# Kernel optimization log

Measured on AMD Instinct MI355X. Metric: run time of the kernel, lower is better.

Reference implementation:

```python
import jax, jax.numpy as jnp
import numpy as np

B, N, F, Tf, Tm, Df, Dm = 8, 128, 128, 64, 256, 32, 128
E, H, TE = 64, 128, 64  # node_emb_dim, hidden_dim, time_emb_dim


def setup_inputs() -> dict:
    key = jax.random.key(0)
    ks = jax.random.split(key, 16)
    s = 0.05
    return {
        'noisy_adj': jax.random.normal(ks[0], (B, N, N), jnp.float32),
        'node_feats': jax.random.normal(ks[1], (B, N, F), jnp.float32),
        'feat_fnirs': jax.random.normal(ks[2], (B, N, Tf, Df), jnp.float32),
        'feat_music': jax.random.normal(ks[3], (B, 1, Tm, Dm), jnp.float32),
        'g_pre': jax.random.normal(ks[4], (B, N, N), jnp.float32),
        'node_W': jax.random.normal(ks[5], (F, E), jnp.float32) * s,
        'node_b': jnp.zeros((E,), jnp.float32),
        'fnirs_W': jax.random.normal(ks[6], (Df, H), jnp.float32) * s,
        'fnirs_b': jnp.zeros((H,), jnp.float32),
        'music_W': jax.random.normal(ks[7], (Dm, H), jnp.float32) * s,
        'music_b': jnp.zeros((H,), jnp.float32),
        'mlp_W1': jax.random.normal(ks[8], (2 * E + 2 + H + TE, H), jnp.float32) * s,
        'mlp_b1': jnp.zeros((H,), jnp.float32),
        'mlp_W2': jax.random.normal(ks[9], (H, 1), jnp.float32) * s,
        'mlp_b2': jnp.zeros((1,), jnp.float32),
        't': jax.random.randint(ks[10], (B,), 0, Tf),
    }


def _time_embedding(t_idx):
    # sinusoidal timestep embedding -> [B, TE]
    half = TE // 2
    inv_freq = jnp.exp(-jnp.arange(half, dtype=jnp.float32) * (jnp.log(10000.0) / (half - 1)))
    freqs = t_idx.astype(jnp.float32)[:, None] * inv_freq  # [B, half]
    return jnp.concatenate([jnp.sin(freqs), jnp.cos(freqs)], axis=-1)


def _conditional(feat_fnirs, feat_music, fnirs_W, fnirs_b, music_W, music_b):
    # cross-attention: fNIRS timesteps attend over music timesteps
    q = feat_fnirs @ fnirs_W + fnirs_b          # [B,N,Tf,H]
    kv = feat_music @ music_W + music_b         # [B,1,Tm,H]
    scale = 1.0 / jnp.sqrt(jnp.float32(H))
    scores = jnp.einsum('bnfh,bomh->bnfm', q, kv) * scale  # [B,N,Tf,Tm]
    attn = jax.nn.softmax(scores, axis=-1)
    ctx = jnp.einsum('bnfm,bomh->bnfh', attn, kv)
    fused = q + ctx                              # [B,N,Tf,H]
    attn_weights = attn.mean(axis=1)             # mean across channels -> [B,Tf,Tm]
    ent = -(attn * jnp.log(attn + 1e-8)).sum(-1)
    attention_loss = ent.mean()
    return fused, attn_weights, attention_loss


def reference(noisy_adj, node_feats, feat_fnirs, feat_music, g_pre,
              node_W, node_b, fnirs_W, fnirs_b, music_W, music_b,
              mlp_W1, mlp_b1, mlp_W2, mlp_b2, t):
    h = node_feats @ node_W + node_b             # [B,N,E]

    fused, attn_weights, attention_loss = _conditional(
        feat_fnirs, feat_music, fnirs_W, fnirs_b, music_W, music_b)

    t_idx = jnp.clip(t, 0, fused.shape[2] - 1)
    # gather conditional state at diffusion step t -> [B,N,H]
    idx = jnp.broadcast_to(t_idx[:, None, None, None], (B, N, 1, H))
    cond_t = jnp.take_along_axis(fused, idx, axis=2)[:, :, 0, :]

    time_emb = _time_embedding(t_idx)            # [B,TE]

    # Fused edge MLP layer-1: split W1 along the concat axis instead of
    # materializing the [B,N,N,in_dim] concat tensor (same math).
    W1_hi = mlp_W1[:E]
    W1_hj = mlp_W1[E:2 * E]
    w_adj = mlp_W1[2 * E]          # [H]
    w_gpre = mlp_W1[2 * E + 1]     # [H]
    W1_cond = mlp_W1[2 * E + 2:2 * E + 2 + H]
    W1_time = mlp_W1[2 * E + 2 + H:]

    pre = ((h @ W1_hi)[:, :, None, :]            # h_i varies over row i
           + (h @ W1_hj)[:, None, :, :]          # h_j varies over col j
           + noisy_adj[..., None] * w_adj
           + g_pre[..., None] * w_gpre
           + (cond_t @ W1_cond)[:, None, :, :]   # cond broadcast over row i
           + (time_emb @ W1_time)[:, None, None, :]
           + mlp_b1)                             # [B,N,N,H]
    hid = jax.nn.relu(pre)
    noise_pred = (hid @ mlp_W2)[..., 0] + mlp_b2[0]  # [B,N,N]
    return noise_pred, attn_weights, attention_loss
```

## Files before the change

### kernel.cpp

```cpp
#include <hip/hip_runtime.h>
#include <hip/hip_bf16.h>

#define Bn  8
#define Nn  128
#define Fn  128
#define Tfn 64
#define Tmn 256
#define Dfn 32
#define Dmn 128
#define En  64
#define Hn  128
#define TEn 64

#define OUT_AW_OFF   (Bn*Nn*Nn)
#define OUT_LOSS_OFF (Bn*Nn*Nn + Bn*Tfn*Tmn)

#define WS_G     0
#define WS_BIAS  32768
#define WS_KVT   34816
#define WS_FWT   165888
#define WS_NWT   167936
#define WS_HIT   172032
#define WS_HJT   176128
#define WS_CONDT 180224
#define WS_TVEC  188416
#define WS_PI    189440
#define WS_PJ    320512
#define WS_LOSS  451584
#define WS_MWT   451588
#define WS_FWB   459780

#define SCALE 0.08838834764831845f

typedef __attribute__((ext_vector_type(8))) short short8;
typedef __attribute__((ext_vector_type(4))) float f32x4;

__device__ __forceinline__ unsigned short f2bf(float x) {
  __hip_bfloat16 h = __float2bfloat16(x);
  return __builtin_bit_cast(unsigned short, h);
}
__device__ __forceinline__ unsigned int pk2(float a, float b) {
  return (unsigned int)f2bf(a) | ((unsigned int)f2bf(b) << 16);
}

__global__ __launch_bounds__(128) void k_wprep(
    const float* __restrict__ W1, const float* __restrict__ b1,
    const float* __restrict__ node_W, const float* __restrict__ fnirs_W,
    const float* __restrict__ fnirs_b, const float* __restrict__ music_W,
    const int* __restrict__ t,
    unsigned short* __restrict__ fwt, unsigned short* __restrict__ nwt,
    unsigned short* __restrict__ hit, unsigned short* __restrict__ hjt,
    unsigned short* __restrict__ condt, unsigned short* __restrict__ mwt,
    unsigned short* __restrict__ fwb, float* __restrict__ tvec,
    float* __restrict__ loss_acc)
{
  int blk = blockIdx.x, tid = threadIdx.x;
  if (blk < 8) {
    int b = blk;
    __shared__ float te_l[TEn];
    if (tid < TEn/2) {
      int tcl = min(max(t[b], 0), Tfn - 1);
      float fr = (float)tcl * __expf(-(float)tid * (logf(10000.f) / (TEn/2 - 1)));
      te_l[tid] = __sinf(fr);
      te_l[tid + TEn/2] = __cosf(fr);
    }
    __syncthreads();
    float a = b1[tid];
    #pragma unroll 8
    for (int u = 0; u < TEn; u++) a = fmaf(te_l[u], W1[(2*En + 2 + Hn + u)*Hn + tid], a);
    tvec[b*Hn + tid] = a;
    if (b == 0 && tid == 0) loss_acc[0] = 0.f;
  } else if (blk < 16) {
    int q = blk - 8;
    #pragma unroll 4
    for (int i = 0; i < 16; i++) {
      int k = q*16 + i;
      condt[k*Hn + tid] = f2bf(W1[(2*En + 2 + tid)*Hn + k]);
    }
  } else if (blk < 20) {
    int q = blk - 16;
    int e = tid & 63, kh = tid >> 6;
    #pragma unroll 4
    for (int i = 0; i < 16; i++) {
      int k = q*32 + kh*16 + i;
      hit[k*En + e] = f2bf(W1[e*Hn + k]);
    }
  } else if (blk < 24) {
    int q = blk - 20;
    int e = tid & 63, kh = tid >> 6;
    #pragma unroll 4
    for (int i = 0; i < 16; i++) {
      int k = q*32 + kh*16 + i;
      hjt[k*En + e] = f2bf(W1[(En + e)*Hn + k]);
    }
  } else if (blk < 32) {
    int q = blk - 24;
    int fl = tid & 15, eh = tid >> 4;
    #pragma unroll 4
    for (int i = 0; i < 8; i++) {
      int e = eh*8 + i;
      nwt[e*Fn + q*16 + fl] = f2bf(node_W[(q*16 + fl)*En + e]);
    }
  } else if (blk < 34) {
    int q = blk - 32;
    int d = tid & 31, hh = tid >> 5;
    #pragma unroll 4
    for (int i = 0; i < 16; i++) {
      int h = q*64 + hh*16 + i;
      fwt[h*Dfn + d] = f2bf(fnirs_W[d*Hn + h]);
    }
  } else if (blk < 36) {
    int q = blk - 34;
    #pragma unroll 4
    for (int i = 0; i < 64; i++) {
      int h = q*64 + i;
      mwt[h*Dmn + tid] = f2bf(music_W[(size_t)tid*Hn + h]);
    }
  } else {
    #pragma unroll 4
    for (int row = 0; row < 48; row++) {
      float v = (row < 32) ? fnirs_W[row*Hn + tid] : (row == 32 ? fnirs_b[tid] : 0.f);
      fwb[row*Hn + tid] = f2bf(v);
    }
  }
}

__global__ __launch_bounds__(256) void k_music(
    const float* __restrict__ feat_music, const float* __restrict__ music_b,
    const unsigned short* __restrict__ mwt, const unsigned short* __restrict__ fwb,
    unsigned short* __restrict__ kvT, unsigned short* __restrict__ G_bf,
    float* __restrict__ bias)
{
  __shared__ unsigned short fm_l[32][136];
  __shared__ unsigned short kv_l[32][136];

  int tid = threadIdx.x;
  int b = blockIdx.x >> 3;
  int m0 = (blockIdx.x & 7) << 5;

  {
    int m = tid >> 3, c = (tid & 7) * 16;
    const float* src = feat_music + ((size_t)b*Tmn + m0 + m)*Dmn + c;
    float4 x0 = ((const float4*)src)[0];
    float4 x1 = ((const float4*)src)[1];
    float4 x2 = ((const float4*)src)[2];
    float4 x3 = ((const float4*)src)[3];
    uint4 pa, pb;
    pa.x = pk2(x0.x, x0.y); pa.y = pk2(x0.z, x0.w);
    pa.z = pk2(x1.x, x1.y); pa.w = pk2(x1.z, x1.w);
    pb.x = pk2(x2.x, x2.y); pb.y = pk2(x2.z, x2.w);
    pb.z = pk2(x3.x, x3.y); pb.w = pk2(x3.z, x3.w);
    uint4* dst = (uint4*)&fm_l[m][c];
    dst[0] = pa; dst[1] = pb;
  }
  __syncthreads();

  int lane = tid & 63, wv = tid >> 6;
  int col = lane & 15, kq = lane >> 4;
  int rt = wv & 1, cp = wv >> 1;

  short8 aF[4];
  #pragma unroll
  for (int ks = 0; ks < 4; ks++)
    aF[ks] = *(const short8*)&fm_l[rt*16 + col][ks*32 + kq*8];

  #pragma unroll
  for (int htl = 0; htl < 4; htl++) {
    int ht = cp*4 + htl;
    int h = ht*16 + col;
    f32x4 acc = {0.f,0.f,0.f,0.f};
    #pragma unroll
    for (int ks = 0; ks < 4; ks++) {
      short8 bfr = *(const short8*)(mwt + (size_t)h*Dmn + ks*32 + kq*8);
      acc = __builtin_amdgcn_mfma_f32_16x16x32_bf16(aF[ks], bfr, acc, 0, 0, 0);
    }
    float mb = music_b[h];
    unsigned short kvb[4];
    #pragma unroll
    for (int r = 0; r < 4; r++) {
      float v = acc[r] + mb;
      kvb[r] = f2bf(v);
      kv_l[rt*16 + kq*4 + r][h] = kvb[r];
    }
    *(ushort4*)(kvT + ((size_t)b*Hn + h)*Tmn + m0 + rt*16 + kq*4) =
        make_ushort4(kvb[0], kvb[1], kvb[2], kvb[3]);
  }
  __syncthreads();

  short8 aK[4];
  #pragma unroll
  for (int ks = 0; ks < 4; ks++)
    aK[ks] = *(const short8*)&kv_l[rt*16 + col][ks*32 + kq*8];

  int nct = (cp == 0) ? 2 : 1;
  for (int cti = 0; cti < nct; cti++) {
    int ct = (cp == 0) ? cti*2 : 1;
    f32x4 acc = {0.f,0.f,0.f,0.f};
    #pragma unroll
    for (int ks = 0; ks < 4; ks++) {
      short8 bfr = *(const short8*)(fwb + (size_t)(ct*16 + col)*Hn + ks*32 + kq*8);
      acc = __builtin_amdgcn_mfma_f32_16x16x32_bf16(aK[ks], bfr, acc, 0, 0, 0);
    }
    if (ct < 2) {
      #pragma unroll
      for (int r = 0; r < 4; r++)
        G_bf[((size_t)b*Tmn + m0 + rt*16 + kq*4 + r)*Dfn + ct*16 + col] =
            f2bf(acc[r] * SCALE);
    } else if (col == 0) {
      #pragma unroll
      for (int r = 0; r < 4; r++)
        bias[(size_t)b*Tmn + m0 + rt*16 + kq*4 + r] = acc[r] * SCALE;
    }
  }
}

struct SmemAttn {
  unsigned short feat_l[Nn][40];
  unsigned short G_l[Tmn][40];
  float bias_l[Tmn];
  float aw_l[4][Tmn];
  float ent_l[4];
};
struct SmemCond {
  unsigned short featT_l[16][40];
  unsigned short A_l[16][264];
  unsigned short nf_l[16][136];
  unsigned short h_l[16][72];
  unsigned short cond_l[16][136];
  float sS[4][16];
  float tvec_l[Hn];
};
union __align__(16) SmemK2 {
  SmemAttn a;
  SmemCond c;
};

__global__ __launch_bounds__(256, 2) void k_attn_cond(
    const float* __restrict__ feat_fnirs, const float* __restrict__ node_feats,
    const float* __restrict__ node_b, const int* __restrict__ t,
    const unsigned short* __restrict__ G_bf, const float* __restrict__ bias,
    const unsigned short* __restrict__ kvT, const unsigned short* __restrict__ fwt,
    const unsigned short* __restrict__ nwt, const unsigned short* __restrict__ hit,
    const unsigned short* __restrict__ hjt, const unsigned short* __restrict__ condt,
    const float* __restrict__ tvec, float* __restrict__ Pi, float* __restrict__ Pj,
    float* __restrict__ aw_out, float* __restrict__ loss_acc)
{
  __shared__ SmemK2 smem;
  int tid = threadIdx.x;
  int lane = tid & 63, wv = tid >> 6;
  int col = lane & 15, kq = lane >> 4;

  if (blockIdx.x < 512) {
    int b = blockIdx.x >> 6, f = blockIdx.x & 63;
    {
      const uint4* gg = (const uint4*)(G_bf + (size_t)b*Tmn*Dfn);
      #pragma unroll
      for (int v0 = 0; v0 < 4; v0++) {
        int v = tid + v0*256;
        uint4 x = gg[v];
        int m = v >> 2, qt = v & 3;
        *((uint4*)&smem.a.G_l[m][qt*8]) = x;
      }
      smem.a.bias_l[tid] = bias[b*Tmn + tid];
      int n = tid >> 1, hf = tid & 1;
      const float* src = feat_fnirs + (((size_t)b*Nn + n)*Tfn + f)*Dfn + hf*16;
      float4 x0 = ((const float4*)src)[0];
      float4 x1 = ((const float4*)src)[1];
      float4 x2 = ((const float4*)src)[2];
      float4 x3 = ((const float4*)src)[3];
      uint4 pa, pb;
      pa.x = pk2(x0.x, x0.y); pa.y = pk2(x0.z, x0.w);
      pa.z = pk2(x1.x, x1.y); pa.w = pk2(x1.z, x1.w);
      pb.x = pk2(x2.x, x2.y); pb.y = pk2(x2.z, x2.w);
      pb.z = pk2(x3.x, x3.y); pb.w = pk2(x3.z, x3.w);
      uint4* dst = (uint4*)&smem.a.feat_l[n][hf*16];
      dst[0] = pa; dst[1] = pb;
    }
    __syncthreads();

    int n0 = wv * 32;
    short8 a0 = *(const short8*)&smem.a.feat_l[n0 + col][kq*8];
    short8 a1 = *(const short8*)&smem.a.feat_l[n0 + 16 + col][kq*8];

    float S0[4] = {0,0,0,0}, S1[4] = {0,0,0,0};
    float T0[4] = {0,0,0,0}, T1[4] = {0,0,0,0};
    float p0[16][4], p1[16][4];

    #pragma unroll
    for (int mt = 0; mt < 16; mt++) {
      short8 bfr = *(const short8*)&smem.a.G_l[mt*16 + col][kq*8];
      float bv = smem.a.bias_l[mt*16 + col];
      f32x4 c0 = __builtin_amdgcn_mfma_f32_16x16x32_bf16(a0, bfr, (f32x4){0.f,0.f,0.f,0.f}, 0, 0, 0);
      f32x4 c1 = __builtin_amdgcn_mfma_f32_16x16x32_bf16(a1, bfr, (f32x4){0.f,0.f,0.f,0.f}, 0, 0, 0);
      #pragma unroll
      for (int r = 0; r < 4; r++) {
        float sc = c0[r] + bv;
        float p = __expf(sc);
        S0[r] += p; T0[r] = fmaf(p, sc, T0[r]); p0[mt][r] = p;
        sc = c1[r] + bv;
        p = __expf(sc);
        S1[r] += p; T1[r] = fmaf(p, sc, T1[r]); p1[mt][r] = p;
      }
    }

    #pragma unroll
    for (int r = 0; r < 4; r++) {
      #pragma unroll
      for (int off = 1; off < 16; off <<= 1) {
        S0[r] += __shfl_xor(S0[r], off);
        S1[r] += __shfl_xor(S1[r], off);
        T0[r] += __shfl_xor(T0[r], off);
        T1[r] += __shfl_xor(T1[r], off);
      }
    }
    float i0v[4], i1v[4];
    #pragma unroll
    for (int r = 0; r < 4; r++) { i0v[r] = 1.f / S0[r]; i1v[r] = 1.f / S1[r]; }

    float ent = 0.f;
    if (col == 0) {
      #pragma unroll
      for (int r = 0; r < 4; r++) {
        ent += (__logf(S0[r]) - T0[r] * i0v[r]);
        ent += (__logf(S1[r]) - T1[r] * i1v[r]);
      }
    }
    ent += __shfl_xor(ent, 32); ent += __shfl_xor(ent, 16);
    ent += __shfl_xor(ent, 8);  ent += __shfl_xor(ent, 4);
    ent += __shfl_xor(ent, 2);  ent += __shfl_xor(ent, 1);
    if (lane == 0) smem.a.ent_l[wv] = ent;

    #pragma unroll
    for (int mt = 0; mt < 16; mt++) {
      float a = 0.f;
      #pragma unroll
      for (int r = 0; r < 4; r++) {
        a = fmaf(p0[mt][r], i0v[r], a);
        a = fmaf(p1[mt][r], i1v[r], a);
      }
      a += __shfl_xor(a, 16);
      a += __shfl_xor(a, 32);
      if (lane < 16) smem.a.aw_l[wv][mt*16 + lane] = a;
    }
    __syncthreads();

    float s = (smem.a.aw_l[0][tid] + smem.a.aw_l[1][tid]) +
              (smem.a.aw_l[2][tid] + smem.a.aw_l[3][tid]);
    aw_out[((size_t)b*Tfn + f)*Tmn + tid] = s * (1.f/(float)Nn);
    if (tid == 0)
      atomicAdd(loss_acc, (smem.a.ent_l[0] + smem.a.ent_l[1]) +
                          (smem.a.ent_l[2] + smem.a.ent_l[3]));
    return;
  }

  int blk = blockIdx.x - 512;
  int b = blk >> 3;
  int i0 = (blk & 7) << 4;
  int tcl = min(max(t[b], 0), Tfn - 1);

  if (tid < 128) {
    int i = tid >> 3, c = (tid & 7) * 4;
    const float* src = feat_fnirs + (((size_t)b*Nn + i0 + i)*Tfn + tcl)*Dfn + c;
    float4 x = *(const float4*)src;
    *(unsigned int*)&smem.c.featT_l[i][c]     = pk2(x.x, x.y);
    *(unsigned int*)&smem.c.featT_l[i][c + 2] = pk2(x.z, x.w);
    smem.c.tvec_l[tid] = tvec[b*Hn + tid];
  }
  {
    int i = tid >> 4, c = (tid & 15) * 8;
    const float* src = node_feats + ((size_t)b*Nn + i0 + i)*Fn + c;
    float4 x0 = ((const float4*)src)[0];
    float4 x1 = ((const float4*)src)[1];
    *(unsigned int*)&smem.c.nf_l[i][c]     = pk2(x0.x, x0.y);
    *(unsigned int*)&smem.c.nf_l[i][c + 2] = pk2(x0.z, x0.w);
    *(unsigned int*)&smem.c.nf_l[i][c + 4] = pk2(x1.x, x1.y);
    *(unsigned int*)&smem.c.nf_l[i][c + 6] = pk2(x1.z, x1.w);
  }
  __syncthreads();

  short8 a_feat = *(const short8*)&smem.c.featT_l[col][kq*8];

  float p[4][4];
  float Sp[4] = {0,0,0,0};
  #pragma unroll
  for (int mtl = 0; mtl < 4; mtl++) {
    int mt = wv*4 + mtl;
    short8 bg = *(const short8*)(G_bf + ((size_t)b*Tmn + mt*16 + col)*Dfn + kq*8);
    f32x4 c = __builtin_amdgcn_mfma_f32_16x16x32_bf16(a_feat, bg, (f32x4){0.f,0.f,0.f,0.f}, 0, 0, 0);
    float bv = bias[b*Tmn + mt*16 + col];
    #pragma unroll
    for (int r = 0; r < 4; r++) {
      float pp = __expf(c[r] + bv);
      p[mtl][r] = pp;
      Sp[r] += pp;
    }
  }
  #pragma unroll
  for (int r = 0; r < 4; r++) {
    float v = Sp[r];
    v += __shfl_xor(v, 1); v += __shfl_xor(v, 2);
    v += __shfl_xor(v, 4); v += __shfl_xor(v, 8);
    Sp[r] = v;
  }
  if (col == 0) {
    #pragma unroll
    for (int r = 0; r < 4; r++) smem.c.sS[wv][kq*4 + r] = Sp[r];
  }
  __syncthreads();
  float invS[4];
  #pragma unroll
  for (int r = 0; r < 4; r++)
    invS[r] = 1.f / (smem.c.sS[0][kq*4+r] + smem.c.sS[1][kq*4+r] +
                     smem.c.sS[2][kq*4+r] + smem.c.sS[3][kq*4+r]);
  #pragma unroll
  for (int mtl = 0; mtl < 4; mtl++) {
    #pragma unroll
    for (int r = 0; r < 4; r++)
      smem.c.A_l[kq*4 + r][(wv*4 + mtl)*16 + col] = f2bf(p[mtl][r] * invS[r]);
  }
  __syncthreads();

  f32x4 accC0 = {0.f,0.f,0.f,0.f}, accC1 = {0.f,0.f,0.f,0.f};
  {
    int ct0 = wv*2, ct1 = wv*2 + 1;
    short8 bq0 = *(const short8*)(fwt + (size_t)(ct0*16 + col)*Dfn + kq*8);
    short8 bq1 = *(const short8*)(fwt + (size_t)(ct1*16 + col)*Dfn + kq*8);
    accC0 = __builtin_amdgcn_mfma_f32_16x16x32_bf16(a_feat, bq0, accC0, 0, 0, 0);
    accC1 = __builtin_amdgcn_mfma_f32_16x16x32_bf16(a_feat, bq1, accC1, 0, 0, 0);
    #pragma unroll
    for (int ks = 0; ks < 8; ks++) {
      short8 aA = *(const short8*)&smem.c.A_l[col][ks*32 + kq*8];
      short8 bk0 = *(const short8*)(kvT + ((size_t)b*Hn + ct0*16 + col)*Tmn + ks*32 + kq*8);
      short8 bk1 = *(const short8*)(kvT + ((size_t)b*Hn + ct1*16 + col)*Tmn + ks*32 + kq*8);
      accC0 = __builtin_amdgcn_mfma_f32_16x16x32_bf16(aA, bk0, accC0, 0, 0, 0);
      accC1 = __builtin_amdgcn_mfma_f32_16x16x32_bf16(aA, bk1, accC1, 0, 0, 0);
    }
  }
  f32x4 accH = {0.f,0.f,0.f,0.f};
  #pragma unroll
  for (int ks = 0; ks < 4; ks++) {
    short8 aN = *(const short8*)&smem.c.nf_l[col][ks*32 + kq*8];
    short8 bn = *(const short8*)(nwt + (size_t)(wv*16 + col)*Fn + ks*32 + kq*8);
    accH = __builtin_amdgcn_mfma_f32_16x16x32_bf16(aN, bn, accH, 0, 0, 0);
  }
  float nb = node_b[wv*16 + col];
  #pragma unroll
  for (int r = 0; r < 4; r++) {
    smem.c.cond_l[kq*4 + r][(wv*2    )*16 + col] = f2bf(accC0[r]);
    smem.c.cond_l[kq*4 + r][(wv*2 + 1)*16 + col] = f2bf(accC1[r]);
    smem.c.h_l[kq*4 + r][wv*16 + col] = f2bf(accH[r] + nb);
  }
  __syncthreads();

  short8 aH[2];
  aH[0] = *(const short8*)&smem.c.h_l[col][kq*8];
  aH[1] = *(const short8*)&smem.c.h_l[col][32 + kq*8];
  #pragma unroll
  for (int ctl = 0; ctl < 2; ctl++) {
    int ct = wv*2 + ctl;
    f32x4 accPi = {0.f,0.f,0.f,0.f}, accPj = {0.f,0.f,0.f,0.f};
    #pragma unroll
    for (int ks = 0; ks < 2; ks++) {
      short8 bi_ = *(const short8*)(hit + (size_t)(ct*16 + col)*En + ks*32 + kq*8);
      short8 bj_ = *(const short8*)(hjt + (size_t)(ct*16 + col)*En + ks*32 + kq*8);
      accPi = __builtin_amdgcn_mfma_f32_16x16x32_bf16(aH[ks], bi_, accPi, 0, 0, 0);
      accPj = __builtin_amdgcn_mfma_f32_16x16x32_bf16(aH[ks], bj_, accPj, 0, 0, 0);
    }
    #pragma unroll
    for (int ks = 0; ks < 4; ks++) {
      short8 aC = *(const short8*)&smem.c.cond_l[col][ks*32 + kq*8];
      short8 bc = *(const short8*)(condt + (size_t)(ct*16 + col)*Hn + ks*32 + kq*8);
      accPj = __builtin_amdgcn_mfma_f32_16x16x32_bf16(aC, bc, accPj, 0, 0, 0);
    }
    float tv = smem.c.tvec_l[ct*16 + col];
    #pragma unroll
    for (int r = 0; r < 4; r++) {
      size_t row = (size_t)b*Nn + i0 + kq*4 + r;
      Pi[row*Hn + ct*16 + col] = accPi[r];
      Pj[row*Hn + ct*16 + col] = accPj[r] + tv;
    }
  }
}

__global__ __launch_bounds__(256) void k_edge(
    const float* __restrict__ adj, const float* __restrict__ gpre,
    const float* __restrict__ W1, const float* __restrict__ W2,
    const float* __restrict__ b2p, const float* __restrict__ Pi,
    const float* __restrict__ Pj, float* __restrict__ out,
    const float* __restrict__ loss_acc)
{
  int b  = blockIdx.x >> 6;
  int ib = (blockIdx.x >> 1) & 31;
  int jh = blockIdx.x & 1;
  int i0 = ib * 4;
  int tid = threadIdx.x;

  __shared__ float4 Pj_s4[64*32];
  __shared__ float4 Pi_s4[4*32];
  __shared__ float4 w2_s[32], wa_s[32], wg_s[32];

  {
    const float4* Pjg = (const float4*)(Pj + ((size_t)b*Nn + jh*64)*Hn);
    #pragma unroll
    for (int v0 = 0; v0 < 8; v0++) {
      int idx = tid + v0*256;
      int j = idx >> 5, c = idx & 31;
      Pj_s4[j*32 + (c ^ (j & 31))] = Pjg[j*32 + c];
    }
    if (tid < 128) {
      int r = tid >> 5, c = tid & 31;
      Pi_s4[r*32 + c] = ((const float4*)(Pi + ((size_t)b*Nn + i0 + r)*Hn))[c];
    } else if (tid < 160) {
      int c = tid - 128;
      w2_s[c] = ((const float4*)W2)[c];
      wa_s[c] = ((const float4*)(W1 + (2*En)*Hn))[c];
      wg_s[c] = ((const float4*)(W1 + (2*En + 1)*Hn))[c];
    }
  }
  __syncthreads();

  int r = tid >> 6, lane = tid & 63;
  int i = i0 + r, j = jh*64 + lane;
  float b2v = b2p[0];
  float adjv = adj [((size_t)b*Nn + i)*Nn + j];
  float gpv  = gpre[((size_t)b*Nn + i)*Nn + j];
  float a0 = 0.f, a1 = 0.f, a2 = 0.f, a3 = 0.f;
  #pragma unroll
  for (int c = 0; c < 32; c++) {
    float4 pj = Pj_s4[lane*32 + (c ^ (lane & 31))];
    float4 pi = Pi_s4[r*32 + c];
    float4 wa = wa_s[c], wg = wg_s[c], w2 = w2_s[c];
    float e0 = pi.x + pj.x + adjv*wa.x + gpv*wg.x;
    float e1 = pi.y + pj.y + adjv*wa.y + gpv*wg.y;
    float e2 = pi.z + pj.z + adjv*wa.z + gpv*wg.z;
    float e3 = pi.w + pj.w + adjv*wa.w + gpv*wg.w;
    a0 = fmaf(fmaxf(e0, 0.f), w2.x, a0);
    a1 = fmaf(fmaxf(e1, 0.f), w2.y, a1);
    a2 = fmaf(fmaxf(e2, 0.f), w2.z, a2);
    a3 = fmaf(fmaxf(e3, 0.f), w2.w, a3);
  }
  out[((size_t)b*Nn + i)*Nn + j] = (a0 + a1) + (a2 + a3) + b2v;

  if (blockIdx.x == 0 && tid == 0)
    out[OUT_LOSS_OFF] = loss_acc[0] * (1.f / (float)(Bn*Nn*Tfn));
}

extern "C" void kernel_launch(void* const* d_in, const int* in_sizes, int n_in,
                              void* d_out, int out_size, void* d_ws, size_t ws_size,
                              hipStream_t stream) {
  (void)in_sizes; (void)n_in; (void)out_size; (void)ws_size;
  const float* noisy_adj  = (const float*)d_in[0];
  const float* node_feats = (const float*)d_in[1];
  const float* feat_fnirs = (const float*)d_in[2];
  const float* feat_music = (const float*)d_in[3];
  const float* g_pre      = (const float*)d_in[4];
  const float* node_W     = (const float*)d_in[5];
  const float* node_b     = (const float*)d_in[6];
  const float* fnirs_W    = (const float*)d_in[7];
  const float* fnirs_b    = (const float*)d_in[8];
  const float* music_W    = (const float*)d_in[9];
  const float* music_b    = (const float*)d_in[10];
  const float* mlp_W1     = (const float*)d_in[11];
  const float* mlp_b1     = (const float*)d_in[12];
  const float* mlp_W2     = (const float*)d_in[13];
  const float* mlp_b2     = (const float*)d_in[14];
  const int*   t          = (const int*)d_in[15];

  float* out = (float*)d_out;
  float* ws = (float*)d_ws;
  unsigned short* g_ws    = (unsigned short*)(ws + WS_G);
  float*          bias_ws = ws + WS_BIAS;
  unsigned short* kvt_ws  = (unsigned short*)(ws + WS_KVT);
  unsigned short* fwt_ws  = (unsigned short*)(ws + WS_FWT);
  unsigned short* nwt_ws  = (unsigned short*)(ws + WS_NWT);
  unsigned short* hit_ws  = (unsigned short*)(ws + WS_HIT);
  unsigned short* hjt_ws  = (unsigned short*)(ws + WS_HJT);
  unsigned short* cndt_ws = (unsigned short*)(ws + WS_CONDT);
  float*          tvec_ws = ws + WS_TVEC;
  float*          Pi_ws   = ws + WS_PI;
  float*          Pj_ws   = ws + WS_PJ;
  float*          loss_ws = ws + WS_LOSS;
  unsigned short* mwt_ws  = (unsigned short*)(ws + WS_MWT);
  unsigned short* fwb_ws  = (unsigned short*)(ws + WS_FWB);

  k_wprep    <<<37,   128, 0, stream>>>(mlp_W1, mlp_b1, node_W, fnirs_W, fnirs_b,
                                        music_W, t, fwt_ws, nwt_ws, hit_ws, hjt_ws,
                                        cndt_ws, mwt_ws, fwb_ws, tvec_ws, loss_ws);
  k_music    <<<64,   256, 0, stream>>>(feat_music, music_b, mwt_ws, fwb_ws,
                                        kvt_ws, g_ws, bias_ws);
  k_attn_cond<<<576,  256, 0, stream>>>(feat_fnirs, node_feats, node_b, t,
                                        g_ws, bias_ws, kvt_ws, fwt_ws, nwt_ws,
                                        hit_ws, hjt_ws, cndt_ws, tvec_ws,
                                        Pi_ws, Pj_ws, out + OUT_AW_OFF, loss_ws);
  k_edge     <<<512,  256, 0, stream>>>(noisy_adj, g_pre, mlp_W1, mlp_W2, mlp_b2,
                                        Pi_ws, Pj_ws, out, loss_ws);
}
```

Before: 136.5 us.

## Fuse all four kernels into one persistent kernel with grid barriers

Replaces the four separate launches (weight prep, music projection, attention/cond, edge MLP) with one 256-block kernel that uses atomic-counter grid barriers between phases. The music and fnirs weight transposes are dropped, and those weights are converted to bf16 on the fly inside the music phase. Each block now loops over two attention units and over later-phase work. This removes launch overhead and the inter-kernel gaps. In exchange it adds spin-wait barriers, which rely on all 256 blocks being co-resident, plus a memset, and there are strided scalar loads of music_W.

```diff
diff --git a/kernel.cpp b/kernel.cpp
--- a/kernel.cpp
+++ b/kernel.cpp
@@ -27,8 +27,6 @@
 #define WS_PI    189440
 #define WS_PJ    320512
 #define WS_LOSS  451584
-#define WS_MWT   451588
-#define WS_FWB   459780
 
 #define SCALE 0.08838834764831845f
 
@@ -43,175 +41,15 @@
   return (unsigned int)f2bf(a) | ((unsigned int)f2bf(b) << 16);
 }
 
-__global__ __launch_bounds__(128) void k_wprep(
-    const float* __restrict__ W1, const float* __restrict__ b1,
-    const float* __restrict__ node_W, const float* __restrict__ fnirs_W,
-    const float* __restrict__ fnirs_b, const float* __restrict__ music_W,
-    const int* __restrict__ t,
-    unsigned short* __restrict__ fwt, unsigned short* __restrict__ nwt,
-    unsigned short* __restrict__ hit, unsigned short* __restrict__ hjt,
-    unsigned short* __restrict__ condt, unsigned short* __restrict__ mwt,
-    unsigned short* __restrict__ fwb, float* __restrict__ tvec,
-    float* __restrict__ loss_acc)
-{
-  int blk = blockIdx.x, tid = threadIdx.x;
-  if (blk < 8) {
-    int b = blk;
-    __shared__ float te_l[TEn];
-    if (tid < TEn/2) {
-      int tcl = min(max(t[b], 0), Tfn - 1);
-      float fr = (float)tcl * __expf(-(float)tid * (logf(10000.f) / (TEn/2 - 1)));
-      te_l[tid] = __sinf(fr);
-      te_l[tid + TEn/2] = __cosf(fr);
-    }
-    __syncthreads();
-    float a = b1[tid];
-    #pragma unroll 8
-    for (int u = 0; u < TEn; u++) a = fmaf(te_l[u], W1[(2*En + 2 + Hn + u)*Hn + tid], a);
-    tvec[b*Hn + tid] = a;
-    if (b == 0 && tid == 0) loss_acc[0] = 0.f;
-  } else if (blk < 16) {
-    int q = blk - 8;
-    #pragma unroll 4
-    for (int i = 0; i < 16; i++) {
-      int k = q*16 + i;
-      condt[k*Hn + tid] = f2bf(W1[(2*En + 2 + tid)*Hn + k]);
-    }
-  } else if (blk < 20) {
-    int q = blk - 16;
-    int e = tid & 63, kh = tid >> 6;
-    #pragma unroll 4
-    for (int i = 0; i < 16; i++) {
-      int k = q*32 + kh*16 + i;
-      hit[k*En + e] = f2bf(W1[e*Hn + k]);
-    }
-  } else if (blk < 24) {
-    int q = blk - 20;
-    int e = tid & 63, kh = tid >> 6;
-    #pragma unroll 4
-    for (int i = 0; i < 16; i++) {
-      int k = q*32 + kh*16 + i;
-      hjt[k*En + e] = f2bf(W1[(En + e)*Hn + k]);
-    }
-  } else if (blk < 32) {
-    int q = blk - 24;
-    int fl = tid & 15, eh = tid >> 4;
-    #pragma unroll 4
-    for (int i = 0; i < 8; i++) {
-      int e = eh*8 + i;
-      nwt[e*Fn + q*16 + fl] = f2bf(node_W[(q*16 + fl)*En + e]);
-    }
-  } else if (blk < 34) {
-    int q = blk - 32;
-    int d = tid & 31, hh = tid >> 5;
-    #pragma unroll 4
-    for (int i = 0; i < 16; i++) {
-      int h = q*64 + hh*16 + i;
-      fwt[h*Dfn + d] = f2bf(fnirs_W[d*Hn + h]);
-    }
-  } else if (blk < 36) {
-    int q = blk - 34;
-    #pragma unroll 4
-    for (int i = 0; i < 64; i++) {
-      int h = q*64 + i;
-      mwt[h*Dmn + tid] = f2bf(music_W[(size_t)tid*Hn + h]);
-    }
-  } else {
-    #pragma unroll 4
-    for (int row = 0; row < 48; row++) {
-      float v = (row < 32) ? fnirs_W[row*Hn + tid] : (row == 32 ? fnirs_b[tid] : 0.f);
-      fwb[row*Hn + tid] = f2bf(v);
-    }
-  }
-}
-
-__global__ __launch_bounds__(256) void k_music(
-    const float* __restrict__ feat_music, const float* __restrict__ music_b,
-    const unsigned short* __restrict__ mwt, const unsigned short* __restrict__ fwb,
-    unsigned short* __restrict__ kvT, unsigned short* __restrict__ G_bf,
-    float* __restrict__ bias)
-{
-  __shared__ unsigned short fm_l[32][136];
-  __shared__ unsigned short kv_l[32][136];
-
-  int tid = threadIdx.x;
-  int b = blockIdx.x >> 3;
-  int m0 = (blockIdx.x & 7) << 5;
-
-  {
-    int m = tid >> 3, c = (tid & 7) * 16;
-    const float* src = feat_music + ((size_t)b*Tmn + m0 + m)*Dmn + c;
-    float4 x0 = ((const float4*)src)[0];
-    float4 x1 = ((const float4*)src)[1];
-    float4 x2 = ((const float4*)src)[2];
-    float4 x3 = ((const float4*)src)[3];
-    uint4 pa, pb;
-    pa.x = pk2(x0.x, x0.y); pa.y = pk2(x0.z, x0.w);
-    pa.z = pk2(x1.x, x1.y); pa.w = pk2(x1.z, x1.w);
-    pb.x = pk2(x2.x, x2.y); pb.y = pk2(x2.z, x2.w);
-    pb.z = pk2(x3.x, x3.y); pb.w = pk2(x3.z, x3.w);
-    uint4* dst = (uint4*)&fm_l[m][c];
-    dst[0] = pa; dst[1] = pb;
+__device__ __forceinline__ void grid_barrier(unsigned int* ctr, unsigned int target) {
+  __syncthreads();
+  __threadfence();
+  if (threadIdx.x == 0) {
+    atomicAdd(ctr, 1u);
+    while (atomicAdd(ctr, 0u) < target) __builtin_amdgcn_s_sleep(8);
   }
   __syncthreads();
-
-  int lane = tid & 63, wv = tid >> 6;
-  int col = lane & 15, kq = lane >> 4;
-  int rt = wv & 1, cp = wv >> 1;
-
-  short8 aF[4];
-  #pragma unroll
-  for (int ks = 0; ks < 4; ks++)
-    aF[ks] = *(const short8*)&fm_l[rt*16 + col][ks*32 + kq*8];
-
-  #pragma unroll
-  for (int htl = 0; htl < 4; htl++) {
-    int ht = cp*4 + htl;
-    int h = ht*16 + col;
-    f32x4 acc = {0.f,0.f,0.f,0.f};
-    #pragma unroll
-    for (int ks = 0; ks < 4; ks++) {
-      short8 bfr = *(const short8*)(mwt + (size_t)h*Dmn + ks*32 + kq*8);
-      acc = __builtin_amdgcn_mfma_f32_16x16x32_bf16(aF[ks], bfr, acc, 0, 0, 0);
-    }
-    float mb = music_b[h];
-    unsigned short kvb[4];
-    #pragma unroll
-    for (int r = 0; r < 4; r++) {
-      float v = acc[r] + mb;
-      kvb[r] = f2bf(v);
-      kv_l[rt*16 + kq*4 + r][h] = kvb[r];
-    }
-    *(ushort4*)(kvT + ((size_t)b*Hn + h)*Tmn + m0 + rt*16 + kq*4) =
-        make_ushort4(kvb[0], kvb[1], kvb[2], kvb[3]);
-  }
-  __syncthreads();
-
-  short8 aK[4];
-  #pragma unroll
-  for (int ks = 0; ks < 4; ks++)
-    aK[ks] = *(const short8*)&kv_l[rt*16 + col][ks*32 + kq*8];
-
-  int nct = (cp == 0) ? 2 : 1;
-  for (int cti = 0; cti < nct; cti++) {
-    int ct = (cp == 0) ? cti*2 : 1;
-    f32x4 acc = {0.f,0.f,0.f,0.f};
-    #pragma unroll
-    for (int ks = 0; ks < 4; ks++) {
-      short8 bfr = *(const short8*)(fwb + (size_t)(ct*16 + col)*Hn + ks*32 + kq*8);
-      acc = __builtin_amdgcn_mfma_f32_16x16x32_bf16(aK[ks], bfr, acc, 0, 0, 0);
-    }
-    if (ct < 2) {
-      #pragma unroll
-      for (int r = 0; r < 4; r++)
-        G_bf[((size_t)b*Tmn + m0 + rt*16 + kq*4 + r)*Dfn + ct*16 + col] =
-            f2bf(acc[r] * SCALE);
-    } else if (col == 0) {
-      #pragma unroll
-      for (int r = 0; r < 4; r++)
-        bias[(size_t)b*Tmn + m0 + rt*16 + kq*4 + r] = acc[r] * SCALE;
-    }
-  }
+  __threadfence();
 }
 
 struct SmemAttn {
@@ -230,28 +68,228 @@
   float sS[4][16];
   float tvec_l[Hn];
 };
-union __align__(16) SmemK2 {
+struct SmemMusic {
+  unsigned short fm_l[32][136];
+  unsigned short kv_l[32][136];
+};
+struct SmemWprep { float te_l[TEn]; };
+struct SmemEdge {
+  float4 Pj_s4[64*32];
+  float4 Pi_s4[4*32];
+  float4 w2_s[32];
+  float4 wa_s[32];
+  float4 wg_s[32];
+};
+union __align__(16) SmemAll {
   SmemAttn a;
   SmemCond c;
+  SmemMusic m;
+  SmemWprep w;
+  SmemEdge e;
 };
 
-__global__ __launch_bounds__(256, 2) void k_attn_cond(
-    const float* __restrict__ feat_fnirs, const float* __restrict__ node_feats,
-    const float* __restrict__ node_b, const int* __restrict__ t,
-    const unsigned short* __restrict__ G_bf, const float* __restrict__ bias,
-    const unsigned short* __restrict__ kvT, const unsigned short* __restrict__ fwt,
-    const unsigned short* __restrict__ nwt, const unsigned short* __restrict__ hit,
-    const unsigned short* __restrict__ hjt, const unsigned short* __restrict__ condt,
-    const float* __restrict__ tvec, float* __restrict__ Pi, float* __restrict__ Pj,
-    float* __restrict__ aw_out, float* __restrict__ loss_acc)
+__global__ __launch_bounds__(256, 2) void k_all(
+    const float* __restrict__ noisy_adj, const float* __restrict__ node_feats,
+    const float* __restrict__ feat_fnirs, const float* __restrict__ feat_music,
+    const float* __restrict__ g_pre, const float* __restrict__ node_W,
+    const float* __restrict__ node_b, const float* __restrict__ fnirs_W,
+    const float* __restrict__ fnirs_b, const float* __restrict__ music_W,
+    const float* __restrict__ music_b, const float* __restrict__ W1,
+    const float* __restrict__ b1, const float* __restrict__ W2,
+    const float* __restrict__ b2p, const int* __restrict__ t,
+    float* __restrict__ out, float* __restrict__ ws)
 {
-  __shared__ SmemK2 smem;
+  __shared__ SmemAll smem;
+
+  unsigned short* G_bf  = (unsigned short*)(ws + WS_G);
+  float*          bias  = ws + WS_BIAS;
+  unsigned short* kvT   = (unsigned short*)(ws + WS_KVT);
+  unsigned short* fwt   = (unsigned short*)(ws + WS_FWT);
+  unsigned short* nwt   = (unsigned short*)(ws + WS_NWT);
+  unsigned short* hit   = (unsigned short*)(ws + WS_HIT);
+  unsigned short* hjt   = (unsigned short*)(ws + WS_HJT);
+  unsigned short* condt = (unsigned short*)(ws + WS_CONDT);
+  float*          tvec  = ws + WS_TVEC;
+  float*          Pi    = ws + WS_PI;
+  float*          Pj    = ws + WS_PJ;
+  float*          loss_acc = ws + WS_LOSS;
+  unsigned int*   bar1  = (unsigned int*)(ws + WS_LOSS + 1);
+  unsigned int*   bar2  = (unsigned int*)(ws + WS_LOSS + 2);
+  float*          aw_out   = out + OUT_AW_OFF;
+
   int tid = threadIdx.x;
+  int blk = blockIdx.x;
   int lane = tid & 63, wv = tid >> 6;
   int col = lane & 15, kq = lane >> 4;
 
-  if (blockIdx.x < 512) {
-    int b = blockIdx.x >> 6, f = blockIdx.x & 63;
+  if (blk < 64) {
+    int b = blk >> 3;
+    int m0 = (blk & 7) << 5;
+    {
+      int m = tid >> 3, c = (tid & 7) * 16;
+      const float* src = feat_music + ((size_t)b*Tmn + m0 + m)*Dmn + c;
+      float4 x0 = ((const float4*)src)[0];
+      float4 x1 = ((const float4*)src)[1];
+      float4 x2 = ((const float4*)src)[2];
+      float4 x3 = ((const float4*)src)[3];
+      uint4 pa, pb;
+      pa.x = pk2(x0.x, x0.y); pa.y = pk2(x0.z, x0.w);
+      pa.z = pk2(x1.x, x1.y); pa.w = pk2(x1.z, x1.w);
+      pb.x = pk2(x2.x, x2.y); pb.y = pk2(x2.z, x2.w);
+      pb.z = pk2(x3.x, x3.y); pb.w = pk2(x3.z, x3.w);
+      uint4* dst = (uint4*)&smem.m.fm_l[m][c];
+      dst[0] = pa; dst[1] = pb;
+    }
+    __syncthreads();
+    int rt = wv & 1, cp = wv >> 1;
+    short8 aF[4];
+    #pragma unroll
+    for (int ks = 0; ks < 4; ks++)
+      aF[ks] = *(const short8*)&smem.m.fm_l[rt*16 + col][ks*32 + kq*8];
+
+    #pragma unroll
+    for (int htl = 0; htl < 4; htl++) {
+      int h = (cp*4 + htl)*16 + col;
+      f32x4 acc = {0.f,0.f,0.f,0.f};
+      #pragma unroll
+      for (int ks = 0; ks < 4; ks++) {
+        int d0 = ks*32 + kq*8;
+        short8 bfr;
+        #pragma unroll
+        for (int j = 0; j < 8; j++)
+          bfr[j] = (short)f2bf(music_W[(size_t)(d0 + j)*Hn + h]);
+        acc = __builtin_amdgcn_mfma_f32_16x16x32_bf16(aF[ks], bfr, acc, 0, 0, 0);
+      }
+      float mb = music_b[h];
+      unsigned short kvb[4];
+      #pragma unroll
+      for (int r = 0; r < 4; r++) {
+        float v = acc[r] + mb;
+        kvb[r] = f2bf(v);
+        smem.m.kv_l[rt*16 + kq*4 + r][h] = kvb[r];
+      }
+      *(ushort4*)(kvT + ((size_t)b*Hn + h)*Tmn + m0 + rt*16 + kq*4) =
+          make_ushort4(kvb[0], kvb[1], kvb[2], kvb[3]);
+    }
+    __syncthreads();
+    short8 aK[4];
+    #pragma unroll
+    for (int ks = 0; ks < 4; ks++)
+      aK[ks] = *(const short8*)&smem.m.kv_l[rt*16 + col][ks*32 + kq*8];
+    int nct = (cp == 0) ? 2 : 1;
+    for (int cti = 0; cti < nct; cti++) {
+      int ct = (cp == 0) ? cti*2 : 1;
+      f32x4 acc = {0.f,0.f,0.f,0.f};
+      #pragma unroll
+      for (int ks = 0; ks < 4; ks++) {
+        int d0 = ks*32 + kq*8;
+        short8 bfr;
+        if (ct < 2) {
+          const float* wr = fnirs_W + (size_t)(ct*16 + col)*Hn + d0;
+          float4 wa = ((const float4*)wr)[0];
+          float4 wb = ((const float4*)wr)[1];
+          uint4 uu;
+          uu.x = pk2(wa.x, wa.y); uu.y = pk2(wa.z, wa.w);
+          uu.z = pk2(wb.x, wb.y); uu.w = pk2(wb.z, wb.w);
+          bfr = __builtin_bit_cast(short8, uu);
+        } else if (col == 0) {
+          const float* wr = fnirs_b + d0;
+          float4 wa = ((const float4*)wr)[0];
+          float4 wb = ((const float4*)wr)[1];
+          uint4 uu;
+          uu.x = pk2(wa.x, wa.y); uu.y = pk2(wa.z, wa.w);
+          uu.z = pk2(wb.x, wb.y); uu.w = pk2(wb.z, wb.w);
+          bfr = __builtin_bit_cast(short8, uu);
+        } else {
+          bfr = (short8){0,0,0,0,0,0,0,0};
+        }
+        acc = __builtin_amdgcn_mfma_f32_16x16x32_bf16(aK[ks], bfr, acc, 0, 0, 0);
+      }
+      if (ct < 2) {
+        #pragma unroll
+        for (int r = 0; r < 4; r++)
+          G_bf[((size_t)b*Tmn + m0 + rt*16 + kq*4 + r)*Dfn + ct*16 + col] =
+              f2bf(acc[r] * SCALE);
+      } else if (col == 0) {
+        #pragma unroll
+        for (int r = 0; r < 4; r++)
+          bias[(size_t)b*Tmn + m0 + rt*16 + kq*4 + r] = acc[r] * SCALE;
+      }
+    }
+  } else if (blk < 98) {
+    int wblk = blk - 64;
+    if (wblk < 8) {
+      int b = wblk;
+      if (tid < TEn/2) {
+        int tcl = min(max(t[b], 0), Tfn - 1);
+        float fr = (float)tcl * __expf(-(float)tid * (logf(10000.f) / (TEn/2 - 1)));
+        smem.w.te_l[tid] = __sinf(fr);
+        smem.w.te_l[tid + TEn/2] = __cosf(fr);
+      }
+      __syncthreads();
+      if (tid < Hn) {
+        float a = b1[tid];
+        #pragma unroll 8
+        for (int u = 0; u < TEn; u++)
+          a = fmaf(smem.w.te_l[u], W1[(2*En + 2 + Hn + u)*Hn + tid], a);
+        tvec[b*Hn + tid] = a;
+      }
+    } else if (wblk < 16) {
+      int q = wblk - 8;
+      if (tid < 128) {
+        #pragma unroll 4
+        for (int i = 0; i < 16; i++) {
+          int k = q*16 + i;
+          condt[k*Hn + tid] = f2bf(W1[(2*En + 2 + tid)*Hn + k]);
+        }
+      }
+    } else if (wblk < 20) {
+      int q = wblk - 16;
+      if (tid < 128) {
+        int e = tid & 63, kh = tid >> 6;
+        #pragma unroll 4
+        for (int i = 0; i < 16; i++) {
+          int k = q*32 + kh*16 + i;
+          hit[k*En + e] = f2bf(W1[e*Hn + k]);
+        }
+      }
+    } else if (wblk < 24) {
+      int q = wblk - 20;
+      if (tid < 128) {
+        int e = tid & 63, kh = tid >> 6;
+        #pragma unroll 4
+        for (int i = 0; i < 16; i++) {
+          int k = q*32 + kh*16 + i;
+          hjt[k*En + e] = f2bf(W1[(En + e)*Hn + k]);
+        }
+      }
+    } else if (wblk < 32) {
+      int q = wblk - 24;
+      if (tid < 128) {
+        int fl = tid & 15, eh = tid >> 4;
+        #pragma unroll 4
+        for (int i = 0; i < 8; i++) {
+          int e = eh*8 + i;
+          nwt[e*Fn + q*16 + fl] = f2bf(node_W[(q*16 + fl)*En + e]);
+        }
+      }
+    } else {
+      int q = wblk - 32;
+      if (tid < 128) {
+        int d = tid & 31, hh = tid >> 5;
+        #pragma unroll 4
+        for (int i = 0; i < 16; i++) {
+          int h = q*64 + hh*16 + i;
+          fwt[h*Dfn + d] = f2bf(fnirs_W[d*Hn + h]);
+        }
+      }
+    }
+  }
+  grid_barrier(bar1, 256);
+
+  for (int u = 0; u < 2; u++) {
+    int unit = blk*2 + u;
+    int b = unit >> 6, f = unit & 63;
     {
       const uint4* gg = (const uint4*)(G_bf + (size_t)b*Tmn*Dfn);
       #pragma unroll
@@ -350,198 +388,191 @@
     if (tid == 0)
       atomicAdd(loss_acc, (smem.a.ent_l[0] + smem.a.ent_l[1]) +
                           (smem.a.ent_l[2] + smem.a.ent_l[3]));
-    return;
+    __syncthreads();
   }
 
-  int blk = blockIdx.x - 512;
-  int b = blk >> 3;
-  int i0 = (blk & 7) << 4;
-  int tcl = min(max(t[b], 0), Tfn - 1);
-
-  if (tid < 128) {
-    int i = tid >> 3, c = (tid & 7) * 4;
-    const float* src = feat_fnirs + (((size_t)b*Nn + i0 + i)*Tfn + tcl)*Dfn + c;
-    float4 x = *(const float4*)src;
-    *(unsigned int*)&smem.c.featT_l[i][c]     = pk2(x.x, x.y);
-    *(unsigned int*)&smem.c.featT_l[i][c + 2] = pk2(x.z, x.w);
-    smem.c.tvec_l[tid] = tvec[b*Hn + tid];
+  if (blk < 64) {
+    int b = blk >> 3;
+    int i0 = (blk & 7) << 4;
+    int tcl = min(max(t[b], 0), Tfn - 1);
+
+    if (tid < 128) {
+      int i = tid >> 3, c = (tid & 7) * 4;
+      const float* src = feat_fnirs + (((size_t)b*Nn + i0 + i)*Tfn + tcl)*Dfn + c;
+      float4 x = *(const float4*)src;
+      *(unsigned int*)&smem.c.featT_l[i][c]     = pk2(x.x, x.y);
+      *(unsigned int*)&smem.c.featT_l[i][c + 2] = pk2(x.z, x.w);
+      smem.c.tvec_l[tid] = tvec[b*Hn + tid];
+    }
+    {
+      int i = tid >> 4, c = (tid & 15) * 8;
+      const float* src = node_feats + ((size_t)b*Nn + i0 + i)*Fn + c;
+      float4 x0 = ((const float4*)src)[0];
+      float4 x1 = ((const float4*)src)[1];
+      *(unsigned int*)&smem.c.nf_l[i][c]     = pk2(x0.x, x0.y);
+      *(unsigned int*)&smem.c.nf_l[i][c + 2] = pk2(x0.z, x0.w);
+      *(unsigned int*)&smem.c.nf_l[i][c + 4] = pk2(x1.x, x1.y);
+      *(unsigned int*)&smem.c.nf_l[i][c + 6] = pk2(x1.z, x1.w);
+    }
+    __syncthreads();
+
+    short8 a_feat = *(const short8*)&smem.c.featT_l[col][kq*8];
+
+    float p[4][4];
+    float Sp[4] = {0,0,0,0};
+    #pragma unroll
+    for (int mtl = 0; mtl < 4; mtl++) {
+      int mt = wv*4 + mtl;
+      short8 bg = *(const short8*)(G_bf + ((size_t)b*Tmn + mt*16 + col)*Dfn + kq*8);
+      f32x4 c = __builtin_amdgcn_mfma_f32_16x16x32_bf16(a_feat, bg, (f32x4){0.f,0.f,0.f,0.f}, 0, 0, 0);
+      float bv = bias[b*Tmn + mt*16 + col];
+      #pragma unroll
+      for (int r = 0; r < 4; r++) {
+        float pp = __expf(c[r] + bv);
+        p[mtl][r] = pp;
+        Sp[r] += pp;
+      }
+    }
+    #pragma unroll
+    for (int r = 0; r < 4; r++) {
+      float v = Sp[r];
+      v += __shfl_xor(v, 1); v += __shfl_xor(v, 2);
+      v += __shfl_xor(v, 4); v += __shfl_xor(v, 8);
+      Sp[r] = v;
+    }
+    if (col == 0) {
+      #pragma unroll
+      for (int r = 0; r < 4; r++) smem.c.sS[wv][kq*4 + r] = Sp[r];
+    }
+    __syncthreads();
+    float invS[4];
+    #pragma unroll
+    for (int r = 0; r < 4; r++)
+      invS[r] = 1.f / (smem.c.sS[0][kq*4+r] + smem.c.sS[1][kq*4+r] +
+                       smem.c.sS[2][kq*4+r] + smem.c.sS[3][kq*4+r]);
+    #pragma unroll
+    for (int mtl = 0; mtl < 4; mtl++) {
+      #pragma unroll
+      for (int r = 0; r < 4; r++)
+        smem.c.A_l[kq*4 + r][(wv*4 + mtl)*16 + col] = f2bf(p[mtl][r] * invS[r]);
+    }
+    __syncthreads();
+
+    f32x4 accC0 = {0.f,0.f,0.f,0.f}, accC1 = {0.f,0.f,0.f,0.f};
+    {
+      int ct0 = wv*2, ct1 = wv*2 + 1;
+      short8 bq0 = *(const short8*)(fwt + (size_t)(ct0*16 + col)*Dfn + kq*8);
+      short8 bq1 = *(const short8*)(fwt + (size_t)(ct1*16 + col)*Dfn + kq*8);
+      accC0 = __builtin_amdgcn_mfma_f32_16x16x32_bf16(a_feat, bq0, accC0, 0, 0, 0);
+      accC1 = __builtin_amdgcn_mfma_f32_16x16x32_bf16(a_feat, bq1, accC1, 0, 0, 0);
+      #pragma unroll
+      for (int ks = 0; ks < 8; ks++) {
+        short8 aA = *(const short8*)&smem.c.A_l[col][ks*32 + kq*8];
+        short8 bk0 = *(const short8*)(kvT + ((size_t)b*Hn + ct0*16 + col)*Tmn + ks*32 + kq*8);
+        short8 bk1 = *(const short8*)(kvT + ((size_t)b*Hn + ct1*16 + col)*Tmn + ks*32 + kq*8);
+        accC0 = __builtin_amdgcn_mfma_f32_16x16x32_bf16(aA, bk0, accC0, 0, 0, 0);
+        accC1 = __builtin_amdgcn_mfma_f32_16x16x32_bf16(aA, bk1, accC1, 0, 0, 0);
+      }
+    }
+    f32x4 accH = {0.f,0.f,0.f,0.f};
+    #pragma unroll
+    for (int ks = 0; ks < 4; ks++) {
+      short8 aN = *(const short8*)&smem.c.nf_l[col][ks*32 + kq*8];
+      short8 bn = *(const short8*)(nwt + (size_t)(wv*16 + col)*Fn + ks*32 + kq*8);
+      accH = __builtin_amdgcn_mfma_f32_16x16x32_bf16(aN, bn, accH, 0, 0, 0);
+    }
+    float nb = node_b[wv*16 + col];
+    #pragma unroll
+    for (int r = 0; r < 4; r++) {
+      smem.c.cond_l[kq*4 + r][(wv*2    )*16 + col] = f2bf(accC0[r]);
+      smem.c.cond_l[kq*4 + r][(wv*2 + 1)*16 + col] = f2bf(accC1[r]);
+      smem.c.h_l[kq*4 + r][wv*16 + col] = f2bf(accH[r] + nb);
+    }
+    __syncthreads();
+
+    short8 aH[2];
+    aH[0] = *(const short8*)&smem.c.h_l[col][kq*8];
+    aH[1] = *(const short8*)&smem.c.h_l[col][32 + kq*8];
+    #pragma unroll
+    for (int ctl = 0; ctl < 2; ctl++) {
+      int ct = wv*2 + ctl;
+      f32x4 accPi = {0.f,0.f,0.f,0.f}, accPj = {0.f,0.f,0.f,0.f};
+      #pragma unroll
+      for (int ks = 0; ks < 2; ks++) {
+        short8 bi_ = *(const short8*)(hit + (size_t)(ct*16 + col)*En + ks*32 + kq*8);
+        short8 bj_ = *(const short8*)(hjt + (size_t)(ct*16 + col)*En + ks*32 + kq*8);
+        accPi = __builtin_amdgcn_mfma_f32_16x16x32_bf16(aH[ks], bi_, accPi, 0, 0, 0);
+        accPj = __builtin_amdgcn_mfma_f32_16x16x32_bf16(aH[ks], bj_, accPj, 0, 0, 0);
+      }
+      #pragma unroll
+      for (int ks = 0; ks < 4; ks++) {
+        short8 aC = *(const short8*)&smem.c.cond_l[col][ks*32 + kq*8];
+        short8 bc = *(const short8*)(condt + (size_t)(ct*16 + col)*Hn + ks*32 + kq*8);
+        accPj = __builtin_amdgcn_mfma_f32_16x16x32_bf16(aC, bc, accPj, 0, 0, 0);
+      }
+      float tv = smem.c.tvec_l[ct*16 + col];
+      #pragma unroll
+      for (int r = 0; r < 4; r++) {
+        size_t row = (size_t)b*Nn + i0 + kq*4 + r;
+        Pi[row*Hn + ct*16 + col] = accPi[r];
+        Pj[row*Hn + ct*16 + col] = accPj[r] + tv;
+      }
+    }
   }
-  {
-    int i = tid >> 4, c = (tid & 15) * 8;
-    const float* src = node_feats + ((size_t)b*Nn + i0 + i)*Fn + c;
-    float4 x0 = ((const float4*)src)[0];
-    float4 x1 = ((const float4*)src)[1];
-    *(unsigned int*)&smem.c.nf_l[i][c]     = pk2(x0.x, x0.y);
-    *(unsigned int*)&smem.c.nf_l[i][c + 2] = pk2(x0.z, x0.w);
-    *(unsigned int*)&smem.c.nf_l[i][c + 4] = pk2(x1.x, x1.y);
-    *(unsigned int*)&smem.c.nf_l[i][c + 6] = pk2(x1.z, x1.w);
+  grid_barrier(bar2, 256);
+
+  for (int u = 0; u < 2; u++) {
+    int unit = blk*2 + u;
+    int b  = unit >> 6;
+    int ib = (unit >> 1) & 31;
+    int jh = unit & 1;
+    int i0 = ib * 4;
+
+    {
+      const float4* Pjg = (const float4*)(Pj + ((size_t)b*Nn + jh*64)*Hn);
+      #pragma unroll
+      for (int v0 = 0; v0 < 8; v0++) {
+        int idx = tid + v0*256;
+        int j = idx >> 5, c = idx & 31;
+        smem.e.Pj_s4[j*32 + (c ^ (j & 31))] = Pjg[j*32 + c];
+      }
+      if (tid < 128) {
+        int r = tid >> 5, c = tid & 31;
+        smem.e.Pi_s4[r*32 + c] = ((const float4*)(Pi + ((size_t)b*Nn + i0 + r)*Hn))[c];
+      } else if (tid < 160) {
+        int c = tid - 128;
+        smem.e.w2_s[c] = ((const float4*)W2)[c];
+        smem.e.wa_s[c] = ((const float4*)(W1 + (2*En)*Hn))[c];
+        smem.e.wg_s[c] = ((const float4*)(W1 + (2*En + 1)*Hn))[c];
+      }
+    }
+    __syncthreads();
+
+    int r = tid >> 6, lane2 = tid & 63;
+    int i = i0 + r, j = jh*64 + lane2;
+    float b2v = b2p[0];
+    float adjv = noisy_adj[((size_t)b*Nn + i)*Nn + j];
+    float gpv  = g_pre    [((size_t)b*Nn + i)*Nn + j];
+    float a0 = 0.f, a1 = 0.f, a2 = 0.f, a3 = 0.f;
+    #pragma unroll
+    for (int c = 0; c < 32; c++) {
+      float4 pj = smem.e.Pj_s4[lane2*32 + (c ^ (lane2 & 31))];
+      float4 pi = smem.e.Pi_s4[r*32 + c];
+      float4 wa = smem.e.wa_s[c], wg = smem.e.wg_s[c], w2 = smem.e.w2_s[c];
+      float e0 = pi.x + pj.x + adjv*wa.x + gpv*wg.x;
+      float e1 = pi.y + pj.y + adjv*wa.y + gpv*wg.y;
+      float e2 = pi.z + pj.z + adjv*wa.z + gpv*wg.z;
+      float e3 = pi.w + pj.w + adjv*wa.w + gpv*wg.w;
+      a0 = fmaf(fmaxf(e0, 0.f), w2.x, a0);
+      a1 = fmaf(fmaxf(e1, 0.f), w2.y, a1);
+      a2 = fmaf(fmaxf(e2, 0.f), w2.z, a2);
+      a3 = fmaf(fmaxf(e3, 0.f), w2.w, a3);
+    }
+    out[((size_t)b*Nn + i)*Nn + j] = (a0 + a1) + (a2 + a3) + b2v;
+    __syncthreads();
   }
-  __syncthreads();
-
-  short8 a_feat = *(const short8*)&smem.c.featT_l[col][kq*8];
-
-  float p[4][4];
-  float Sp[4] = {0,0,0,0};
-  #pragma unroll
-  for (int mtl = 0; mtl < 4; mtl++) {
-    int mt = wv*4 + mtl;
-    short8 bg = *(const short8*)(G_bf + ((size_t)b*Tmn + mt*16 + col)*Dfn + kq*8);
-    f32x4 c = __builtin_amdgcn_mfma_f32_16x16x32_bf16(a_feat, bg, (f32x4){0.f,0.f,0.f,0.f}, 0, 0, 0);
-    float bv = bias[b*Tmn + mt*16 + col];
-    #pragma unroll
-    for (int r = 0; r < 4; r++) {
-      float pp = __expf(c[r] + bv);
-      p[mtl][r] = pp;
-      Sp[r] += pp;
-    }
-  }
-  #pragma unroll
-  for (int r = 0; r < 4; r++) {
-    float v = Sp[r];
-    v += __shfl_xor(v, 1); v += __shfl_xor(v, 2);
-    v += __shfl_xor(v, 4); v += __shfl_xor(v, 8);
-    Sp[r] = v;
-  }
-  if (col == 0) {
-    #pragma unroll
-    for (int r = 0; r < 4; r++) smem.c.sS[wv][kq*4 + r] = Sp[r];
-  }
-  __syncthreads();
-  float invS[4];
-  #pragma unroll
-  for (int r = 0; r < 4; r++)
-    invS[r] = 1.f / (smem.c.sS[0][kq*4+r] + smem.c.sS[1][kq*4+r] +
-                     smem.c.sS[2][kq*4+r] + smem.c.sS[3][kq*4+r]);
-  #pragma unroll
-  for (int mtl = 0; mtl < 4; mtl++) {
-    #pragma unroll
-    for (int r = 0; r < 4; r++)
-      smem.c.A_l[kq*4 + r][(wv*4 + mtl)*16 + col] = f2bf(p[mtl][r] * invS[r]);
-  }
-  __syncthreads();
-
-  f32x4 accC0 = {0.f,0.f,0.f,0.f}, accC1 = {0.f,0.f,0.f,0.f};
-  {
-    int ct0 = wv*2, ct1 = wv*2 + 1;
-    short8 bq0 = *(const short8*)(fwt + (size_t)(ct0*16 + col)*Dfn + kq*8);
-    short8 bq1 = *(const short8*)(fwt + (size_t)(ct1*16 + col)*Dfn + kq*8);
-    accC0 = __builtin_amdgcn_mfma_f32_16x16x32_bf16(a_feat, bq0, accC0, 0, 0, 0);
-    accC1 = __builtin_amdgcn_mfma_f32_16x16x32_bf16(a_feat, bq1, accC1, 0, 0, 0);
-    #pragma unroll
-    for (int ks = 0; ks < 8; ks++) {
-      short8 aA = *(const short8*)&smem.c.A_l[col][ks*32 + kq*8];
-      short8 bk0 = *(const short8*)(kvT + ((size_t)b*Hn + ct0*16 + col)*Tmn + ks*32 + kq*8);
-      short8 bk1 = *(const short8*)(kvT + ((size_t)b*Hn + ct1*16 + col)*Tmn + ks*32 + kq*8);
-      accC0 = __builtin_amdgcn_mfma_f32_16x16x32_bf16(aA, bk0, accC0, 0, 0, 0);
-      accC1 = __builtin_amdgcn_mfma_f32_16x16x32_bf16(aA, bk1, accC1, 0, 0, 0);
-    }
-  }
-  f32x4 accH = {0.f,0.f,0.f,0.f};
-  #pragma unroll
-  for (int ks = 0; ks < 4; ks++) {
-    short8 aN = *(const short8*)&smem.c.nf_l[col][ks*32 + kq*8];
-    short8 bn = *(const short8*)(nwt + (size_t)(wv*16 + col)*Fn + ks*32 + kq*8);
-    accH = __builtin_amdgcn_mfma_f32_16x16x32_bf16(aN, bn, accH, 0, 0, 0);
-  }
-  float nb = node_b[wv*16 + col];
-  #pragma unroll
-  for (int r = 0; r < 4; r++) {
-    smem.c.cond_l[kq*4 + r][(wv*2    )*16 + col] = f2bf(accC0[r]);
-    smem.c.cond_l[kq*4 + r][(wv*2 + 1)*16 + col] = f2bf(accC1[r]);
-    smem.c.h_l[kq*4 + r][wv*16 + col] = f2bf(accH[r] + nb);
-  }
-  __syncthreads();
-
-  short8 aH[2];
-  aH[0] = *(const short8*)&smem.c.h_l[col][kq*8];
-  aH[1] = *(const short8*)&smem.c.h_l[col][32 + kq*8];
-  #pragma unroll
-  for (int ctl = 0; ctl < 2; ctl++) {
-    int ct = wv*2 + ctl;
-    f32x4 accPi = {0.f,0.f,0.f,0.f}, accPj = {0.f,0.f,0.f,0.f};
-    #pragma unroll
-    for (int ks = 0; ks < 2; ks++) {
-      short8 bi_ = *(const short8*)(hit + (size_t)(ct*16 + col)*En + ks*32 + kq*8);
-      short8 bj_ = *(const short8*)(hjt + (size_t)(ct*16 + col)*En + ks*32 + kq*8);
-      accPi = __builtin_amdgcn_mfma_f32_16x16x32_bf16(aH[ks], bi_, accPi, 0, 0, 0);
-      accPj = __builtin_amdgcn_mfma_f32_16x16x32_bf16(aH[ks], bj_, accPj, 0, 0, 0);
-    }
-    #pragma unroll
-    for (int ks = 0; ks < 4; ks++) {
-      short8 aC = *(const short8*)&smem.c.cond_l[col][ks*32 + kq*8];
-      short8 bc = *(const short8*)(condt + (size_t)(ct*16 + col)*Hn + ks*32 + kq*8);
-      accPj = __builtin_amdgcn_mfma_f32_16x16x32_bf16(aC, bc, accPj, 0, 0, 0);
-    }
-    float tv = smem.c.tvec_l[ct*16 + col];
-    #pragma unroll
-    for (int r = 0; r < 4; r++) {
-      size_t row = (size_t)b*Nn + i0 + kq*4 + r;
-      Pi[row*Hn + ct*16 + col] = accPi[r];
-      Pj[row*Hn + ct*16 + col] = accPj[r] + tv;
-    }
-  }
-}
-
-__global__ __launch_bounds__(256) void k_edge(
-    const float* __restrict__ adj, const float* __restrict__ gpre,
-    const float* __restrict__ W1, const float* __restrict__ W2,
-    const float* __restrict__ b2p, const float* __restrict__ Pi,
-    const float* __restrict__ Pj, float* __restrict__ out,
-    const float* __restrict__ loss_acc)
-{
-  int b  = blockIdx.x >> 6;
-  int ib = (blockIdx.x >> 1) & 31;
-  int jh = blockIdx.x & 1;
-  int i0 = ib * 4;
-  int tid = threadIdx.x;
-
-  __shared__ float4 Pj_s4[64*32];
-  __shared__ float4 Pi_s4[4*32];
-  __shared__ float4 w2_s[32], wa_s[32], wg_s[32];
-
-  {
-    const float4* Pjg = (const float4*)(Pj + ((size_t)b*Nn + jh*64)*Hn);
-    #pragma unroll
-    for (int v0 = 0; v0 < 8; v0++) {
-      int idx = tid + v0*256;
-      int j = idx >> 5, c = idx & 31;
-      Pj_s4[j*32 + (c ^ (j & 31))] = Pjg[j*32 + c];
-    }
-    if (tid < 128) {
-      int r = tid >> 5, c = tid & 31;
-      Pi_s4[r*32 + c] = ((const float4*)(Pi + ((size_t)b*Nn + i0 + r)*Hn))[c];
-    } else if (tid < 160) {
-      int c = tid - 128;
-      w2_s[c] = ((const float4*)W2)[c];
-      wa_s[c] = ((const float4*)(W1 + (2*En)*Hn))[c];
-      wg_s[c] = ((const float4*)(W1 + (2*En + 1)*Hn))[c];
-    }
-  }
-  __syncthreads();
-
-  int r = tid >> 6, lane = tid & 63;
-  int i = i0 + r, j = jh*64 + lane;
-  float b2v = b2p[0];
-  float adjv = adj [((size_t)b*Nn + i)*Nn + j];
-  float gpv  = gpre[((size_t)b*Nn + i)*Nn + j];
-  float a0 = 0.f, a1 = 0.f, a2 = 0.f, a3 = 0.f;
-  #pragma unroll
-  for (int c = 0; c < 32; c++) {
-    float4 pj = Pj_s4[lane*32 + (c ^ (lane & 31))];
-    float4 pi = Pi_s4[r*32 + c];
-    float4 wa = wa_s[c], wg = wg_s[c], w2 = w2_s[c];
-    float e0 = pi.x + pj.x + adjv*wa.x + gpv*wg.x;
-    float e1 = pi.y + pj.y + adjv*wa.y + gpv*wg.y;
-    float e2 = pi.z + pj.z + adjv*wa.z + gpv*wg.z;
-    float e3 = pi.w + pj.w + adjv*wa.w + gpv*wg.w;
-    a0 = fmaf(fmaxf(e0, 0.f), w2.x, a0);
-    a1 = fmaf(fmaxf(e1, 0.f), w2.y, a1);
-    a2 = fmaf(fmaxf(e2, 0.f), w2.z, a2);
-    a3 = fmaf(fmaxf(e3, 0.f), w2.w, a3);
-  }
-  out[((size_t)b*Nn + i)*Nn + j] = (a0 + a1) + (a2 + a3) + b2v;
-
-  if (blockIdx.x == 0 && tid == 0)
+
+  if (blk == 0 && tid == 0)
     out[OUT_LOSS_OFF] = loss_acc[0] * (1.f / (float)(Bn*Nn*Tfn));
 }
 
@@ -567,31 +598,12 @@
   const int*   t          = (const int*)d_in[15];
 
   float* out = (float*)d_out;
-  float* ws = (float*)d_ws;
-  unsigned short* g_ws    = (unsigned short*)(ws + WS_G);
-  float*          bias_ws = ws + WS_BIAS;
-  unsigned short* kvt_ws  = (unsigned short*)(ws + WS_KVT);
-  unsigned short* fwt_ws  = (unsigned short*)(ws + WS_FWT);
-  unsigned short* nwt_ws  = (unsigned short*)(ws + WS_NWT);
-  unsigned short* hit_ws  = (unsigned short*)(ws + WS_HIT);
-  unsigned short* hjt_ws  = (unsigned short*)(ws + WS_HJT);
-  unsigned short* cndt_ws = (unsigned short*)(ws + WS_CONDT);
-  float*          tvec_ws = ws + WS_TVEC;
-  float*          Pi_ws   = ws + WS_PI;
-  float*          Pj_ws   = ws + WS_PJ;
-  float*          loss_ws = ws + WS_LOSS;
-  unsigned short* mwt_ws  = (unsigned short*)(ws + WS_MWT);
-  unsigned short* fwb_ws  = (unsigned short*)(ws + WS_FWB);
-
-  k_wprep    <<<37,   128, 0, stream>>>(mlp_W1, mlp_b1, node_W, fnirs_W, fnirs_b,
-                                        music_W, t, fwt_ws, nwt_ws, hit_ws, hjt_ws,
-                                        cndt_ws, mwt_ws, fwb_ws, tvec_ws, loss_ws);
-  k_music    <<<64,   256, 0, stream>>>(feat_music, music_b, mwt_ws, fwb_ws,
-                                        kvt_ws, g_ws, bias_ws);
-  k_attn_cond<<<576,  256, 0, stream>>>(feat_fnirs, node_feats, node_b, t,
-                                        g_ws, bias_ws, kvt_ws, fwt_ws, nwt_ws,
-                                        hit_ws, hjt_ws, cndt_ws, tvec_ws,
-                                        Pi_ws, Pj_ws, out + OUT_AW_OFF, loss_ws);
-  k_edge     <<<512,  256, 0, stream>>>(noisy_adj, g_pre, mlp_W1, mlp_W2, mlp_b2,
-                                        Pi_ws, Pj_ws, out, loss_ws);
+  float* ws  = (float*)d_ws;
+
+  hipMemsetAsync((char*)d_ws + (size_t)WS_LOSS * 4, 0, 12, stream);
+
+  k_all<<<256, 256, 0, stream>>>(noisy_adj, node_feats, feat_fnirs, feat_music,
+                                 g_pre, node_W, node_b, fnirs_W, fnirs_b,
+                                 music_W, music_b, mlp_W1, mlp_b1, mlp_W2,
+                                 mlp_b2, t, out, ws);
 }
```

Result: slower. 216.6 us (+58.6%).
